# Kernel optimization log

Hardware: AMD Instinct MI355X
Metric: run time of the kernel (lower is better)

The kernel has to match this reference:

```python
import jax, jax.numpy as jnp
import numpy as np

B, S, D, H = 2, 2048, 1024, 16
HS = D // H
SCALE = 1.0 / float(np.sqrt(HS))


def setup_inputs() -> dict:
    key = jax.random.key(0)
    ks = jax.random.split(key, 11)
    w_std = 1.0 / float(np.sqrt(D))  # ~ nn.Linear init scale
    inp = {
        "queries": jax.random.normal(ks[0], (B, S, D), dtype=jnp.float32),
        "keys": jax.random.normal(ks[1], (B, S, D), dtype=jnp.float32),
        "values": jax.random.normal(ks[2], (B, S, D), dtype=jnp.float32),
        "Wq": jax.random.normal(ks[3], (D, D), dtype=jnp.float32) * w_std,
        "bq": jax.random.normal(ks[4], (D,), dtype=jnp.float32) * w_std,
        "Wk": jax.random.normal(ks[5], (D, D), dtype=jnp.float32) * w_std,
        "bk": jax.random.normal(ks[6], (D,), dtype=jnp.float32) * w_std,
        "Wv": jax.random.normal(ks[7], (D, D), dtype=jnp.float32) * w_std,
        "bv": jax.random.normal(ks[8], (D,), dtype=jnp.float32) * w_std,
        "Wo": jax.random.normal(ks[9], (D, D), dtype=jnp.float32) * w_std,
        "bo": jax.random.normal(ks[10], (D,), dtype=jnp.float32) * w_std,
    }
    return inp


def _split_heads(x):
    # (B,S,D) -> (B,H,S,HS)
    return x.reshape(B, S, H, HS).transpose(0, 2, 1, 3)


def reference(queries, keys, values, Wq, bq, Wk, bk, Wv, bv, Wo, bo):
    # nn.Linear: y = x @ W^T + b
    q = _split_heads(queries @ Wq.T + bq)
    k = _split_heads(keys @ Wk.T + bk)
    v = _split_heads(values @ Wv.T + bv)

    scores = jnp.einsum("bhqd,bhkd->bhqk", q, k) * SCALE  # (B,H,S,S)
    causal = jnp.tril(jnp.ones((S, S), dtype=bool))
    scores = jnp.where(causal, scores, jnp.float32(-1e9))  # masked_fill(-1e9)
    attn = jax.nn.softmax(scores, axis=-1)

    attended = jnp.einsum("bhqk,bhkd->bhqd", attn, v)  # (B,H,S,HS)
    # Faithful to original: .view(B, -1, H*HS) on the contiguous (B,H,S,HS)
    # tensor WITHOUT transposing heads back -> plain row-major reshape.
    outputs = attended.reshape(B, S, H * HS)
    return outputs @ Wo.T + bo
```

## Files before the change

kernel.cpp:

```cpp
#include <hip/hip_runtime.h>
#include <hip/hip_bf16.h>

typedef unsigned short u16;
typedef unsigned int   u32;
typedef __attribute__((ext_vector_type(8))) short bf16x8;
typedef __attribute__((ext_vector_type(4))) float f32x4;
typedef __attribute__((ext_vector_type(4))) float f4v;
typedef __attribute__((ext_vector_type(4))) u16  u16x4;

#define BB 2
#define SS 2048
#define DD 1024
#define HH 16
#define ATT_SCALE 0.125f

__device__ __forceinline__ u16 f2bf(float f) {
  union { float f; u32 u; } c; c.f = f;
  u32 u = c.u + 0x7fffu + ((c.u >> 16) & 1u);
  return (u16)(u >> 16);
}

__device__ __forceinline__ void gload_lds16(const void* g, void* l) {
  __builtin_amdgcn_global_load_lds(
      (const __attribute__((address_space(1))) u32*)g,
      (__attribute__((address_space(3))) u32*)l, 16, 0, 0);
}

__global__ void cvt_bf16_kernel(const float* __restrict__ s0, const float* __restrict__ s1,
                                const float* __restrict__ s2, const float* __restrict__ s3,
                                u16* __restrict__ d0, u16* __restrict__ d1,
                                u16* __restrict__ d2, u16* __restrict__ d3, int n4) {
  const int z = blockIdx.y;
  const float* s = (z == 0) ? s0 : (z == 1) ? s1 : (z == 2) ? s2 : s3;
  u16* d = (z == 0) ? d0 : (z == 1) ? d1 : (z == 2) ? d2 : d3;
  int i = blockIdx.x * blockDim.x + threadIdx.x;
  int stride = gridDim.x * blockDim.x;
  for (int k = i; k < n4; k += stride) {
    f4v v = ((const f4v*)s)[k];
    u16x4 o;
    o[0] = f2bf(v[0]); o[1] = f2bf(v[1]); o[2] = f2bf(v[2]); o[3] = f2bf(v[3]);
    ((u16x4*)d)[k] = o;
  }
}

template<int OUT_F32>
__global__ __launch_bounds__(256, 4) void gemm_bt_kernel(
    const u16* __restrict__ A0, const u16* __restrict__ A1, const u16* __restrict__ A2,
    const u16* __restrict__ W0, const u16* __restrict__ W1, const u16* __restrict__ W2,
    const float* __restrict__ b0, const float* __restrict__ b1, const float* __restrict__ b2,
    void* __restrict__ C0, void* __restrict__ C1, void* __restrict__ C2,
    int M, int N, int K) {
  const int z = blockIdx.z;
  const u16* A = (z == 0) ? A0 : (z == 1) ? A1 : A2;
  const u16* W = (z == 0) ? W0 : (z == 1) ? W1 : W2;
  const float* bias = (z == 0) ? b0 : (z == 1) ? b1 : b2;
  void* Cp = (z == 0) ? C0 : (z == 1) ? C1 : C2;

  __shared__ u16 As[128 * 32];
  __shared__ u16 Bs[64 * 32];
  const int t = threadIdx.x;
  const int lane = t & 63, w = t >> 6;
  const int wr = w >> 1, wc = w & 1;
  const int l15 = lane & 15, l4 = lane >> 4;
  const int m0 = blockIdx.x * 128, n0 = blockIdx.y * 64;

  f32x4 acc[4][2];
#pragma unroll
  for (int m = 0; m < 4; ++m)
#pragma unroll
    for (int n = 0; n < 2; ++n) acc[m][n] = (f32x4)(0.0f);

  const int kc = (t & 3) * 8;
  const int nk = K >> 5;
  for (int kt = 0; kt < nk; ++kt) {
    __syncthreads();
#pragma unroll
    for (int i = 0; i < 2; ++i) {
      int row = (i * 256 + t) >> 2;
      gload_lds16(A + (size_t)(m0 + row) * K + kt * 32 + kc, &As[i * 2048 + w * 512]);
    }
    {
      int row = t >> 2;
      gload_lds16(W + (size_t)(n0 + row) * K + kt * 32 + kc, &Bs[w * 512]);
    }
    __syncthreads();
    bf16x8 af[4], bfr[2];
#pragma unroll
    for (int m = 0; m < 4; ++m) af[m] = *(const bf16x8*)&As[(wr * 64 + m * 16 + l15) * 32 + l4 * 8];
#pragma unroll
    for (int n = 0; n < 2; ++n) bfr[n] = *(const bf16x8*)&Bs[(wc * 32 + n * 16 + l15) * 32 + l4 * 8];
#pragma unroll
    for (int m = 0; m < 4; ++m)
#pragma unroll
      for (int n = 0; n < 2; ++n)
        acc[m][n] = __builtin_amdgcn_mfma_f32_16x16x32_bf16(af[m], bfr[n], acc[m][n], 0, 0, 0);
  }

  float bv[2];
#pragma unroll
  for (int n = 0; n < 2; ++n) bv[n] = bias[n0 + wc * 32 + n * 16 + l15];
#pragma unroll
  for (int m = 0; m < 4; ++m) {
#pragma unroll
    for (int j = 0; j < 4; ++j) {
      int r = m0 + wr * 64 + m * 16 + l4 * 4 + j;
#pragma unroll
      for (int n = 0; n < 2; ++n) {
        int cc = n0 + wc * 32 + n * 16 + l15;
        float v = acc[m][n][j] + bv[n];
        if (OUT_F32) ((float*)Cp)[(size_t)r * N + cc] = v;
        else         ((u16*)Cp)[(size_t)r * N + cc] = f2bf(v);
      }
    }
  }
}

__global__ __launch_bounds__(256, 3) void attn_kernel(
    const u16* __restrict__ Qb, const u16* __restrict__ Kb,
    const u16* __restrict__ Vb, u16* __restrict__ Xb) {
  __shared__ u16 Kl[64 * 72];
  __shared__ u16 Vt[64 * 72];
  __shared__ u16 Pl[64 * 72];

  const int qt = (int)gridDim.x - 1 - (int)blockIdx.x;
  const int bh = blockIdx.y;
  const int b = bh >> 4, h = bh & 15;
  const int q0 = qt * 64;
  const int t = threadIdx.x;
  const int lane = t & 63, w = t >> 6;
  const int l15 = lane & 15, l4 = lane >> 4;

  bf16x8 aq[2];
#pragma unroll
  for (int kf = 0; kf < 2; ++kf)
    aq[kf] = *(const bf16x8*)&Qb[((size_t)b * SS + q0 + w * 16 + l15) * DD +
                                 h * 64 + kf * 32 + l4 * 8];

  f32x4 acc[4];
  float mrun[4], lrun[4];
#pragma unroll
  for (int x = 0; x < 4; ++x) {
    acc[x] = (f32x4)(0.0f);
    mrun[x] = -3.0e38f;
    lrun[x] = 0.0f;
  }

  auto prefetch = [&](int kt, bf16x8* kr, bf16x8* vr) {
#pragma unroll
    for (int i = 0; i < 2; ++i) {
      int c = i * 256 + t;
      size_t goff = ((size_t)b * SS + kt * 64 + (c >> 3)) * DD + h * 64 + (c & 7) * 8;
      kr[i] = *(const bf16x8*)&Kb[goff];
      vr[i] = *(const bf16x8*)&Vb[goff];
    }
  };

  auto stage_write = [&](const bf16x8* kr, const bf16x8* vr) {
#pragma unroll
    for (int i = 0; i < 2; ++i) {
      int c = i * 256 + t;
      int r = c >> 3, d0 = (c & 7) * 8;
      *(bf16x8*)&Kl[r * 72 + d0] = kr[i];
      int rsw = r ^ ((c & 7) << 3);
#pragma unroll
      for (int jj = 0; jj < 8; ++jj)
        Vt[(d0 + jj) * 72 + rsw] = (u16)vr[i][jj];
    }
  };

  auto compute = [&](int kt) {
    const int k0 = kt * 64;
    f32x4 s[4];
#pragma unroll
    for (int nf = 0; nf < 4; ++nf) s[nf] = (f32x4)(0.0f);
#pragma unroll
    for (int nf = 0; nf < 4; ++nf)
#pragma unroll
      for (int kf = 0; kf < 2; ++kf) {
        bf16x8 bk = *(const bf16x8*)&Kl[(nf * 16 + l15) * 72 + kf * 32 + l4 * 8];
        s[nf] = __builtin_amdgcn_mfma_f32_16x16x32_bf16(aq[kf], bk, s[nf], 0, 0, 0);
      }

    const bool need_mask = (k0 + 63 > q0 + w * 16);
#pragma unroll
    for (int nf = 0; nf < 4; ++nf)
#pragma unroll
      for (int j = 0; j < 4; ++j) {
        float v = s[nf][j] * ATT_SCALE;
        if (need_mask) {
          int key = k0 + nf * 16 + l15;
          int qrow = q0 + w * 16 + l4 * 4 + j;
          if (key > qrow) v = -1.0e9f;
        }
        s[nf][j] = v;
      }

#pragma unroll
    for (int j = 0; j < 4; ++j) {
      float v = fmaxf(fmaxf(s[0][j], s[1][j]), fmaxf(s[2][j], s[3][j]));
      v = fmaxf(v, __shfl_xor(v, 1));
      v = fmaxf(v, __shfl_xor(v, 2));
      v = fmaxf(v, __shfl_xor(v, 4));
      v = fmaxf(v, __shfl_xor(v, 8));
      float mnew = fmaxf(mrun[j], v);
      float sc = __expf(mrun[j] - mnew);
      mrun[j] = mnew;
      float sum = 0.0f;
#pragma unroll
      for (int nf = 0; nf < 4; ++nf) {
        float p = __expf(s[nf][j] - mnew);
        s[nf][j] = p;
        sum += p;
      }
      sum += __shfl_xor(sum, 1);
      sum += __shfl_xor(sum, 2);
      sum += __shfl_xor(sum, 4);
      sum += __shfl_xor(sum, 8);
      lrun[j] = lrun[j] * sc + sum;
#pragma unroll
      for (int nd = 0; nd < 4; ++nd) acc[nd][j] *= sc;
    }

#pragma unroll
    for (int nf = 0; nf < 4; ++nf)
#pragma unroll
      for (int j = 0; j < 4; ++j)
        Pl[(w * 16 + l4 * 4 + j) * 72 + nf * 16 + l15] = f2bf(s[nf][j]);

    bf16x8 ap[2];
#pragma unroll
    for (int kf = 0; kf < 2; ++kf)
      ap[kf] = *(const bf16x8*)&Pl[(w * 16 + l15) * 72 + kf * 32 + l4 * 8];
#pragma unroll
    for (int nd = 0; nd < 4; ++nd) {
      int dv = nd * 16 + l15;
      int xr = ((dv >> 3) & 7) << 3;
#pragma unroll
      for (int kf = 0; kf < 2; ++kf) {
        bf16x8 bvf = *(const bf16x8*)&Vt[dv * 72 + ((kf * 32 + l4 * 8) ^ xr)];
        acc[nd] = __builtin_amdgcn_mfma_f32_16x16x32_bf16(ap[kf], bvf, acc[nd], 0, 0, 0);
      }
    }
  };

  const int nkt = qt + 1;
  bf16x8 krA[2], vrA[2], krB[2], vrB[2];
  prefetch(0, krA, vrA);
  for (int kt = 0; kt < nkt;) {
    __syncthreads();
    stage_write(krA, vrA);
    if (kt + 1 < nkt) prefetch(kt + 1, krB, vrB);
    __syncthreads();
    compute(kt);
    ++kt;
    if (kt >= nkt) break;
    __syncthreads();
    stage_write(krB, vrB);
    if (kt + 1 < nkt) prefetch(kt + 1, krA, vrA);
    __syncthreads();
    compute(kt);
    ++kt;
  }

#pragma unroll
  for (int j = 0; j < 4; ++j) {
    float inv = 1.0f / lrun[j];
    int srow = q0 + w * 16 + l4 * 4 + j;
    size_t base = (size_t)b * SS * DD + (size_t)h * SS * 64 + (size_t)srow * 64;
#pragma unroll
    for (int nd = 0; nd < 4; ++nd)
      Xb[base + nd * 16 + l15] = f2bf(acc[nd][j] * inv);
  }
}

extern "C" void kernel_launch(void* const* d_in, const int* in_sizes, int n_in,
                              void* d_out, int out_size, void* d_ws, size_t ws_size,
                              hipStream_t stream) {
  const float* q_in = (const float*)d_in[0];
  const float* k_in = (const float*)d_in[1];
  const float* v_in = (const float*)d_in[2];
  const float* Wq = (const float*)d_in[3];
  const float* bq = (const float*)d_in[4];
  const float* Wk = (const float*)d_in[5];
  const float* bk = (const float*)d_in[6];
  const float* Wv = (const float*)d_in[7];
  const float* bv = (const float*)d_in[8];
  const float* Wo = (const float*)d_in[9];
  const float* bo = (const float*)d_in[10];

  char* ws = (char*)d_ws;
  const size_t SZ_IN = (size_t)BB * SS * DD * 2;
  const size_t SZ_W = (size_t)DD * DD * 2;
  u16* qb  = (u16*)(ws);
  u16* kb  = (u16*)(ws + SZ_IN);
  u16* vb  = (u16*)(ws + 2 * SZ_IN);
  u16* wqb = (u16*)(ws + 3 * SZ_IN);
  u16* wkb = (u16*)(ws + 3 * SZ_IN + SZ_W);
  u16* wvb = (u16*)(ws + 3 * SZ_IN + 2 * SZ_W);
  u16* wob = (u16*)(ws + 3 * SZ_IN + 3 * SZ_W);
  u16* Qb  = (u16*)(ws + 3 * SZ_IN + 4 * SZ_W);
  u16* Kb  = (u16*)(ws + 4 * SZ_IN + 4 * SZ_W);
  u16* Vb  = (u16*)(ws + 5 * SZ_IN + 4 * SZ_W);
  u16* Xb  = (u16*)(ws + 6 * SZ_IN + 4 * SZ_W);

  cvt_bf16_kernel<<<dim3(2048, 3), 256, 0, stream>>>(q_in, k_in, v_in, nullptr,
                                                     qb, kb, vb, nullptr, (BB * SS * DD) / 4);
  cvt_bf16_kernel<<<dim3(1024, 4), 256, 0, stream>>>(Wq, Wk, Wv, Wo,
                                                     wqb, wkb, wvb, wob, (DD * DD) / 4);

  gemm_bt_kernel<0><<<dim3(32, 16, 3), 256, 0, stream>>>(
      qb, kb, vb, wqb, wkb, wvb, bq, bk, bv, Qb, Kb, Vb, BB * SS, DD, DD);

  attn_kernel<<<dim3(SS / 64, BB * HH), 256, 0, stream>>>(Qb, Kb, Vb, Xb);

  gemm_bt_kernel<1><<<dim3(32, 16, 1), 256, 0, stream>>>(
      Xb, Xb, Xb, wob, wob, wob, bo, bo, bo, d_out, d_out, d_out, BB * SS, DD, DD);
}
```

Measured before the change: 319.6 us.

## Produce transposed V from GEMM, drop attention LDS staging, double-buffer GEMM

The V projection is now computed as Wv·vᵀ, so V lands already transposed (head-dim major, tokens contiguous). The attention kernel then reads K and Vᵀ fragments straight from global memory into registers, with no shared-memory staging or block barriers, and keeps only a small per-wave P buffer. It also raises the occupancy hint and adds s_setprio around the MFMA sections. The projection GEMM gains a K=64 double-buffered, XOR-swizzled LDS pipeline and supports a per-row bias. The cost is redundant global and L2 traffic, because each wave refetches K and V on its own instead of sharing staged tiles.

```diff
diff --git a/kernel.cpp b/kernel.cpp
--- a/kernel.cpp
+++ b/kernel.cpp
@@ -12,6 +12,7 @@
 #define SS 2048
 #define DD 1024
 #define HH 16
+#define NT 4096
 #define ATT_SCALE 0.125f
 
 __device__ __forceinline__ u16 f2bf(float f) {
@@ -43,21 +44,21 @@
   }
 }
 
-template<int OUT_F32>
-__global__ __launch_bounds__(256, 4) void gemm_bt_kernel(
-    const u16* __restrict__ A0, const u16* __restrict__ A1, const u16* __restrict__ A2,
-    const u16* __restrict__ W0, const u16* __restrict__ W1, const u16* __restrict__ W2,
-    const float* __restrict__ b0, const float* __restrict__ b1, const float* __restrict__ b2,
-    void* __restrict__ C0, void* __restrict__ C1, void* __restrict__ C2,
+template<int OUT_F32, int BIAS_ROW>
+__global__ __launch_bounds__(256, 3) void gemm_bt_kernel(
+    const u16* __restrict__ A0, const u16* __restrict__ A1,
+    const u16* __restrict__ W0, const u16* __restrict__ W1,
+    const float* __restrict__ bias0, const float* __restrict__ bias1,
+    void* __restrict__ C0, void* __restrict__ C1,
     int M, int N, int K) {
   const int z = blockIdx.z;
-  const u16* A = (z == 0) ? A0 : (z == 1) ? A1 : A2;
-  const u16* W = (z == 0) ? W0 : (z == 1) ? W1 : W2;
-  const float* bias = (z == 0) ? b0 : (z == 1) ? b1 : b2;
-  void* Cp = (z == 0) ? C0 : (z == 1) ? C1 : C2;
-
-  __shared__ u16 As[128 * 32];
-  __shared__ u16 Bs[64 * 32];
+  const u16* A = z ? A1 : A0;
+  const u16* W = z ? W1 : W0;
+  const float* bias = z ? bias1 : bias0;
+  void* Cp = z ? C1 : C0;
+
+  __shared__ u16 As[2][128 * 64];
+  __shared__ u16 Bs[2][64 * 64];
   const int t = threadIdx.x;
   const int lane = t & 63, w = t >> 6;
   const int wr = w >> 1, wc = w & 1;
@@ -70,44 +71,74 @@
 #pragma unroll
     for (int n = 0; n < 2; ++n) acc[m][n] = (f32x4)(0.0f);
 
-  const int kc = (t & 3) * 8;
-  const int nk = K >> 5;
+  const u16* aSrc[4];
+  const u16* bSrc[2];
+#pragma unroll
+  for (int i = 0; i < 4; ++i) {
+    int c = i * 256 + t, row = c >> 3, gg = (c & 7) ^ (row & 7);
+    aSrc[i] = A + (size_t)(m0 + row) * K + gg * 8;
+  }
+#pragma unroll
+  for (int i = 0; i < 2; ++i) {
+    int c = i * 256 + t, row = c >> 3, gg = (c & 7) ^ (row & 7);
+    bSrc[i] = W + (size_t)(n0 + row) * K + gg * 8;
+  }
+
+  auto stage = [&](int buf, int kt) {
+#pragma unroll
+    for (int i = 0; i < 4; ++i)
+      gload_lds16(aSrc[i] + kt * 64, &As[buf][i * 2048 + w * 512]);
+#pragma unroll
+    for (int i = 0; i < 2; ++i)
+      gload_lds16(bSrc[i] + kt * 64, &Bs[buf][i * 2048 + w * 512]);
+  };
+
+  stage(0, 0);
+  __syncthreads();
+
+  const int nk = K >> 6;
   for (int kt = 0; kt < nk; ++kt) {
+    const int cur = kt & 1;
+    if (kt + 1 < nk) stage(cur ^ 1, kt + 1);
+    bf16x8 af[4][2], bfr[2][2];
+#pragma unroll
+    for (int m = 0; m < 4; ++m) {
+      int row = wr * 64 + m * 16 + l15;
+#pragma unroll
+      for (int kf = 0; kf < 2; ++kf)
+        af[m][kf] = *(const bf16x8*)&As[cur][row * 64 + ((kf * 4 + l4) ^ (row & 7)) * 8];
+    }
+#pragma unroll
+    for (int n = 0; n < 2; ++n) {
+      int row = wc * 32 + n * 16 + l15;
+#pragma unroll
+      for (int kf = 0; kf < 2; ++kf)
+        bfr[n][kf] = *(const bf16x8*)&Bs[cur][row * 64 + ((kf * 4 + l4) ^ (row & 7)) * 8];
+    }
+#pragma unroll
+    for (int kf = 0; kf < 2; ++kf)
+#pragma unroll
+      for (int m = 0; m < 4; ++m)
+#pragma unroll
+        for (int n = 0; n < 2; ++n)
+          acc[m][n] = __builtin_amdgcn_mfma_f32_16x16x32_bf16(af[m][kf], bfr[n][kf], acc[m][n], 0, 0, 0);
     __syncthreads();
-#pragma unroll
-    for (int i = 0; i < 2; ++i) {
-      int row = (i * 256 + t) >> 2;
-      gload_lds16(A + (size_t)(m0 + row) * K + kt * 32 + kc, &As[i * 2048 + w * 512]);
-    }
-    {
-      int row = t >> 2;
-      gload_lds16(W + (size_t)(n0 + row) * K + kt * 32 + kc, &Bs[w * 512]);
-    }
-    __syncthreads();
-    bf16x8 af[4], bfr[2];
-#pragma unroll
-    for (int m = 0; m < 4; ++m) af[m] = *(const bf16x8*)&As[(wr * 64 + m * 16 + l15) * 32 + l4 * 8];
-#pragma unroll
-    for (int n = 0; n < 2; ++n) bfr[n] = *(const bf16x8*)&Bs[(wc * 32 + n * 16 + l15) * 32 + l4 * 8];
-#pragma unroll
-    for (int m = 0; m < 4; ++m)
-#pragma unroll
-      for (int n = 0; n < 2; ++n)
-        acc[m][n] = __builtin_amdgcn_mfma_f32_16x16x32_bf16(af[m], bfr[n], acc[m][n], 0, 0, 0);
-  }
-
-  float bv[2];
-#pragma unroll
-  for (int n = 0; n < 2; ++n) bv[n] = bias[n0 + wc * 32 + n * 16 + l15];
+  }
+
+  float bvc[2];
+#pragma unroll
+  for (int n = 0; n < 2; ++n)
+    bvc[n] = BIAS_ROW ? 0.0f : bias[n0 + wc * 32 + n * 16 + l15];
 #pragma unroll
   for (int m = 0; m < 4; ++m) {
 #pragma unroll
     for (int j = 0; j < 4; ++j) {
       int r = m0 + wr * 64 + m * 16 + l4 * 4 + j;
+      float br = BIAS_ROW ? bias[r] : 0.0f;
 #pragma unroll
       for (int n = 0; n < 2; ++n) {
         int cc = n0 + wc * 32 + n * 16 + l15;
-        float v = acc[m][n][j] + bv[n];
+        float v = acc[m][n][j] + (BIAS_ROW ? br : bvc[n]);
         if (OUT_F32) ((float*)Cp)[(size_t)r * N + cc] = v;
         else         ((u16*)Cp)[(size_t)r * N + cc] = f2bf(v);
       }
@@ -115,12 +146,10 @@
   }
 }
 
-__global__ __launch_bounds__(256, 3) void attn_kernel(
+__global__ __launch_bounds__(256, 4) void attn_kernel(
     const u16* __restrict__ Qb, const u16* __restrict__ Kb,
-    const u16* __restrict__ Vb, u16* __restrict__ Xb) {
-  __shared__ u16 Kl[64 * 72];
-  __shared__ u16 Vt[64 * 72];
-  __shared__ u16 Pl[64 * 72];
+    const u16* __restrict__ VtT, u16* __restrict__ Xb) {
+  __shared__ u16 Pl[4][16 * 72];
 
   const int qt = (int)gridDim.x - 1 - (int)blockIdx.x;
   const int bh = blockIdx.y;
@@ -136,6 +165,10 @@
     aq[kf] = *(const bf16x8*)&Qb[((size_t)b * SS + q0 + w * 16 + l15) * DD +
                                  h * 64 + kf * 32 + l4 * 8];
 
+  const u16* Kbase = Kb + (size_t)b * SS * DD + h * 64;
+  const u16* Vbase = VtT + (size_t)h * 64 * NT + (size_t)b * SS;
+  u16* myP = &Pl[w][0];
+
   f32x4 acc[4];
   float mrun[4], lrun[4];
 #pragma unroll
@@ -145,41 +178,30 @@
     lrun[x] = 0.0f;
   }
 
-  auto prefetch = [&](int kt, bf16x8* kr, bf16x8* vr) {
-#pragma unroll
-    for (int i = 0; i < 2; ++i) {
-      int c = i * 256 + t;
-      size_t goff = ((size_t)b * SS + kt * 64 + (c >> 3)) * DD + h * 64 + (c & 7) * 8;
-      kr[i] = *(const bf16x8*)&Kb[goff];
-      vr[i] = *(const bf16x8*)&Vb[goff];
-    }
-  };
-
-  auto stage_write = [&](const bf16x8* kr, const bf16x8* vr) {
-#pragma unroll
-    for (int i = 0; i < 2; ++i) {
-      int c = i * 256 + t;
-      int r = c >> 3, d0 = (c & 7) * 8;
-      *(bf16x8*)&Kl[r * 72 + d0] = kr[i];
-      int rsw = r ^ ((c & 7) << 3);
-#pragma unroll
-      for (int jj = 0; jj < 8; ++jj)
-        Vt[(d0 + jj) * 72 + rsw] = (u16)vr[i][jj];
-    }
-  };
-
-  auto compute = [&](int kt) {
+  for (int kt = 0; kt <= qt; ++kt) {
     const int k0 = kt * 64;
+
     f32x4 s[4];
 #pragma unroll
     for (int nf = 0; nf < 4; ++nf) s[nf] = (f32x4)(0.0f);
-#pragma unroll
-    for (int nf = 0; nf < 4; ++nf)
-#pragma unroll
-      for (int kf = 0; kf < 2; ++kf) {
-        bf16x8 bk = *(const bf16x8*)&Kl[(nf * 16 + l15) * 72 + kf * 32 + l4 * 8];
-        s[nf] = __builtin_amdgcn_mfma_f32_16x16x32_bf16(aq[kf], bk, s[nf], 0, 0, 0);
-      }
+    __builtin_amdgcn_s_setprio(1);
+#pragma unroll
+    for (int nf = 0; nf < 4; ++nf) {
+      const u16* kr = Kbase + (size_t)(k0 + nf * 16 + l15) * DD + l4 * 8;
+      bf16x8 kf0 = *(const bf16x8*)kr;
+      bf16x8 kf1 = *(const bf16x8*)(kr + 32);
+      s[nf] = __builtin_amdgcn_mfma_f32_16x16x32_bf16(aq[0], kf0, s[nf], 0, 0, 0);
+      s[nf] = __builtin_amdgcn_mfma_f32_16x16x32_bf16(aq[1], kf1, s[nf], 0, 0, 0);
+    }
+    __builtin_amdgcn_s_setprio(0);
+
+    bf16x8 vf[4][2];
+#pragma unroll
+    for (int nd = 0; nd < 4; ++nd) {
+      const u16* vr = Vbase + (size_t)(nd * 16 + l15) * NT + k0 + l4 * 8;
+      vf[nd][0] = *(const bf16x8*)vr;
+      vf[nd][1] = *(const bf16x8*)(vr + 32);
+    }
 
     const bool need_mask = (k0 + 63 > q0 + w * 16);
 #pragma unroll
@@ -225,41 +247,20 @@
     for (int nf = 0; nf < 4; ++nf)
 #pragma unroll
       for (int j = 0; j < 4; ++j)
-        Pl[(w * 16 + l4 * 4 + j) * 72 + nf * 16 + l15] = f2bf(s[nf][j]);
+        myP[(l4 * 4 + j) * 72 + nf * 16 + l15] = f2bf(s[nf][j]);
 
     bf16x8 ap[2];
 #pragma unroll
     for (int kf = 0; kf < 2; ++kf)
-      ap[kf] = *(const bf16x8*)&Pl[(w * 16 + l15) * 72 + kf * 32 + l4 * 8];
-#pragma unroll
-    for (int nd = 0; nd < 4; ++nd) {
-      int dv = nd * 16 + l15;
-      int xr = ((dv >> 3) & 7) << 3;
-#pragma unroll
-      for (int kf = 0; kf < 2; ++kf) {
-        bf16x8 bvf = *(const bf16x8*)&Vt[dv * 72 + ((kf * 32 + l4 * 8) ^ xr)];
-        acc[nd] = __builtin_amdgcn_mfma_f32_16x16x32_bf16(ap[kf], bvf, acc[nd], 0, 0, 0);
-      }
-    }
-  };
-
-  const int nkt = qt + 1;
-  bf16x8 krA[2], vrA[2], krB[2], vrB[2];
-  prefetch(0, krA, vrA);
-  for (int kt = 0; kt < nkt;) {
-    __syncthreads();
-    stage_write(krA, vrA);
-    if (kt + 1 < nkt) prefetch(kt + 1, krB, vrB);
-    __syncthreads();
-    compute(kt);
-    ++kt;
-    if (kt >= nkt) break;
-    __syncthreads();
-    stage_write(krB, vrB);
-    if (kt + 1 < nkt) prefetch(kt + 1, krA, vrA);
-    __syncthreads();
-    compute(kt);
-    ++kt;
+      ap[kf] = *(const bf16x8*)&myP[l15 * 72 + kf * 32 + l4 * 8];
+
+    __builtin_amdgcn_s_setprio(1);
+#pragma unroll
+    for (int nd = 0; nd < 4; ++nd)
+#pragma unroll
+      for (int kf = 0; kf < 2; ++kf)
+        acc[nd] = __builtin_amdgcn_mfma_f32_16x16x32_bf16(ap[kf], vf[nd][kf], acc[nd], 0, 0, 0);
+    __builtin_amdgcn_s_setprio(0);
   }
 
 #pragma unroll
@@ -300,7 +301,7 @@
   u16* wob = (u16*)(ws + 3 * SZ_IN + 3 * SZ_W);
   u16* Qb  = (u16*)(ws + 3 * SZ_IN + 4 * SZ_W);
   u16* Kb  = (u16*)(ws + 4 * SZ_IN + 4 * SZ_W);
-  u16* Vb  = (u16*)(ws + 5 * SZ_IN + 4 * SZ_W);
+  u16* VtT = (u16*)(ws + 5 * SZ_IN + 4 * SZ_W);
   u16* Xb  = (u16*)(ws + 6 * SZ_IN + 4 * SZ_W);
 
   cvt_bf16_kernel<<<dim3(2048, 3), 256, 0, stream>>>(q_in, k_in, v_in, nullptr,
@@ -308,11 +309,14 @@
   cvt_bf16_kernel<<<dim3(1024, 4), 256, 0, stream>>>(Wq, Wk, Wv, Wo,
                                                      wqb, wkb, wvb, wob, (DD * DD) / 4);
 
-  gemm_bt_kernel<0><<<dim3(32, 16, 3), 256, 0, stream>>>(
-      qb, kb, vb, wqb, wkb, wvb, bq, bk, bv, Qb, Kb, Vb, BB * SS, DD, DD);
-
-  attn_kernel<<<dim3(SS / 64, BB * HH), 256, 0, stream>>>(Qb, Kb, Vb, Xb);
-
-  gemm_bt_kernel<1><<<dim3(32, 16, 1), 256, 0, stream>>>(
-      Xb, Xb, Xb, wob, wob, wob, bo, bo, bo, d_out, d_out, d_out, BB * SS, DD, DD);
-}
+  gemm_bt_kernel<0, 0><<<dim3(32, 16, 2), 256, 0, stream>>>(
+      qb, kb, wqb, wkb, bq, bk, Qb, Kb, NT, DD, DD);
+
+  gemm_bt_kernel<0, 1><<<dim3(8, 64, 1), 256, 0, stream>>>(
+      wvb, wvb, vb, vb, bv, bv, VtT, VtT, DD, NT, DD);
+
+  attn_kernel<<<dim3(SS / 64, BB * HH), 256, 0, stream>>>(Qb, Kb, VtT, Xb);
+
+  gemm_bt_kernel<1, 0><<<dim3(32, 16, 1), 256, 0, stream>>>(
+      Xb, Xb, wob, wob, bo, bo, d_out, d_out, NT, DD, DD);
+}
```

After: 412.4 us. 29.0% more time.
